# Kernel tuning notes

Hardware: AMD Instinct MI355X
Metric: run time of the kernel (lower is better)

The kernel has to match this reference:

```python
import jax, jax.numpy as jnp
import numpy as np
from jax.scipy.special import ndtri

NUM_BITS = 4
BLOCK_SIZE = 64
OUT_F, IN_F = 4096, 4096


def _nf_table(num_bits=NUM_BITS):
    # Faithful to NFQuantizer.create_normal_map (asymmetric branch)
    offset = 0.9677083
    variations = 2 ** num_bits
    v1 = ndtri(jnp.linspace(offset, 0.5, variations // 2 + 1, dtype=jnp.float32)[:-1])
    v3 = -ndtri(jnp.linspace(offset, 0.5, variations // 2, dtype=jnp.float32)[:-1])
    v = jnp.concatenate([v1, jnp.zeros((1,), jnp.float32), v3])
    v = jnp.sort(v)
    return v / v.max()


def setup_inputs() -> dict:
    key = jax.random.key(0)
    k1, k2, k3, k4, k5 = jax.random.split(key, 5)
    x = jax.random.normal(k1, (8192, IN_F), dtype=jnp.float32)
    qweight = jax.random.randint(k2, (IN_F * OUT_F // 2, 1), 0, 256, dtype=jnp.int32)
    absmax = jax.random.uniform(k3, (IN_F * OUT_F // BLOCK_SIZE, 1), dtype=jnp.float32) * 0.1 + 1e-3
    lora_A = jax.random.normal(k4, (64, IN_F), dtype=jnp.float32) * 0.02
    lora_B = jax.random.normal(k5, (OUT_F, 64), dtype=jnp.float32) * 0.02
    return {"x": x, "qweight": qweight, "absmax": absmax, "lora_A": lora_A, "lora_B": lora_B}


def reference(x, qweight, absmax, lora_A, lora_B):
    table = _nf_table()
    q = qweight[:, 0]
    # dequantize_block: low nibble first (i=0), then high nibble (i=1)
    idx = jnp.stack([q & 0xF, (q >> NUM_BITS) & 0xF], axis=-1)  # [Q, 2]
    w = table[idx].reshape(-1, BLOCK_SIZE) * absmax             # [n_blocks, block_size]
    w = w.reshape(OUT_F, IN_F)
    dense = x @ w.T
    lora = (x @ lora_A.T) @ lora_B.T
    return dense + lora
```

## Files before the change

### kernel.cpp

```cpp
#include <hip/hip_runtime.h>

#define IN_F 4096
#define OUT_F 4096
#define M_ROWS 8192
#define GK 4096

typedef float  floatx4 __attribute__((ext_vector_type(4)));
typedef short  shortx8 __attribute__((ext_vector_type(8)));

__device__ __forceinline__ unsigned short f2bf(float f) {
    unsigned int u = __float_as_uint(f);
    u = (u + 0x7FFFu + ((u >> 16) & 1u)) >> 16;
    return (unsigned short)u;
}

__device__ __forceinline__ float bf2f(unsigned short u) {
    return __uint_as_float((unsigned)u << 16);
}

__constant__ float NF4_TAB[16] = {
    -1.0f, -0.6961928009986877f, -0.5250730514526367f, -0.39491748809814453f,
    -0.28444138169288635f, -0.18477343022823334f, -0.09105003625154495f, 0.0f,
    0.07958029955625534f, 0.16093020141124725f, 0.2461123913526535f, 0.33791524171829224f,
    0.44070982933044434f, 0.5626170039176941f, 0.7229568362236023f, 1.0f
};

__device__ __forceinline__ void gll16(const void* g, void* l) {
    __builtin_amdgcn_global_load_lds(
        (const __attribute__((address_space(1))) void*)g,
        (__attribute__((address_space(3))) void*)l, 16, 0, 0);
}

__global__ __launch_bounds__(256) void prep(
    const float* __restrict__ A, const float* __restrict__ Bm,
    const float* __restrict__ x,
    short* __restrict__ At, short* __restrict__ Bb, short* __restrict__ Xb)
{
    __shared__ float tile[64][65];
    const int b = blockIdx.x;
    const int t = threadIdx.x;

    if (b < 64) {
        const int ib = b * 64;
        const int r = t >> 2, c0 = (t & 3) * 16;
        #pragma unroll
        for (int k = 0; k < 4; ++k) {
            float4 v = *(const float4*)(A + (size_t)r * IN_F + ib + c0 + k * 4);
            tile[r][c0 + k * 4 + 0] = v.x;
            tile[r][c0 + k * 4 + 1] = v.y;
            tile[r][c0 + k * 4 + 2] = v.z;
            tile[r][c0 + k * 4 + 3] = v.w;
        }
        __syncthreads();
        const int i = t >> 2, r0 = (t & 3) * 16;
        union { unsigned short u[8]; int4 v; } p0, p1;
        #pragma unroll
        for (int k = 0; k < 8; ++k) p0.u[k] = f2bf(tile[r0 + k][i]);
        #pragma unroll
        for (int k = 0; k < 8; ++k) p1.u[k] = f2bf(tile[r0 + 8 + k][i]);
        *(int4*)(At + (size_t)(ib + i) * 64 + r0)     = p0.v;
        *(int4*)(At + (size_t)(ib + i) * 64 + r0 + 8) = p1.v;
    } else if (b < 192) {
        const size_t i = ((size_t)(b - 64) * 256 + t) * 8;
        float4 a = *(const float4*)(Bm + i);
        float4 c = *(const float4*)(Bm + i + 4);
        union { unsigned short u[8]; int4 v; } p;
        p.u[0] = f2bf(a.x); p.u[1] = f2bf(a.y); p.u[2] = f2bf(a.z); p.u[3] = f2bf(a.w);
        p.u[4] = f2bf(c.x); p.u[5] = f2bf(c.y); p.u[6] = f2bf(c.z); p.u[7] = f2bf(c.w);
        *(int4*)(Bb + i) = p.v;
    } else {
        const size_t i = ((size_t)(b - 192) * 256 + t) * 8;
        float4 a = *(const float4*)(x + i);
        float4 c = *(const float4*)(x + i + 4);
        union { unsigned short u[8]; int4 v; } p;
        p.u[0] = f2bf(a.x); p.u[1] = f2bf(a.y); p.u[2] = f2bf(a.z); p.u[3] = f2bf(a.w);
        p.u[4] = f2bf(c.x); p.u[5] = f2bf(c.y); p.u[6] = f2bf(c.z); p.u[7] = f2bf(c.w);
        *(int4*)(Xb + i) = p.v;
    }
}

#define BM 128
#define BN 128

__global__ __launch_bounds__(256) void lora_weff(
    const short* __restrict__ Bb,
    const short* __restrict__ At,
    const int*   __restrict__ qw,
    const float* __restrict__ absmax,
    short*       __restrict__ W)
{
    __shared__ union SMem {
        struct { short As[BM * 32]; short Bs[BN * 32]; } mm;
        short Wt[128 * 136];
    } sm;
    __shared__ float nf4s[16];

    const int tid  = threadIdx.x;
    const int lane = tid & 63;
    const int wave = tid >> 6;
    const int bn = blockIdx.x * BN;
    const int bm = blockIdx.y * BM;

    if (tid < 16) nf4s[tid] = NF4_TAB[tid];

    const int r_o = tid >> 1;
    const int h   = tid & 1;
    const int go  = bm + r_o;
    const int* qbase = qw + (size_t)go * 2048 + (bn >> 1) + h * 32;
    int4 q4[8];
    #pragma unroll
    for (int k = 0; k < 8; ++k) q4[k] = *(const int4*)(qbase + 4 * k);
    const float am = absmax[(size_t)go * 64 + (bn >> 6) + h];

    const int ar = tid >> 2;
    const int ac = ((tid & 3) ^ ((ar >> 1) & 3)) * 8;
    const short* gA0 = Bb + (size_t)(bm + ar) * 64 + ac;
    const short* gA1 = gA0 + (size_t)64 * 64;
    const short* gB0 = At + (size_t)(bn + ar) * 64 + ac;
    const short* gB1 = gB0 + (size_t)64 * 64;
    short* lA0 = sm.mm.As + tid * 8;
    short* lA1 = sm.mm.As + 2048 + tid * 8;
    short* lB0 = sm.mm.Bs + tid * 8;
    short* lB1 = sm.mm.Bs + 2048 + tid * 8;

    const int wm = (wave >> 1) * 64;
    const int wn = (wave & 1) * 64;
    const int fr = lane & 15;
    const int qd = lane >> 4;
    const int fk_sw = (((lane >> 4) ^ ((fr >> 1) & 3))) * 8;

    floatx4 zero = {0.f, 0.f, 0.f, 0.f};
    floatx4 acc[4][4];
    #pragma unroll
    for (int i = 0; i < 4; ++i)
        #pragma unroll
        for (int j = 0; j < 4; ++j) acc[i][j] = zero;

    #pragma unroll
    for (int kt = 0; kt < 2; ++kt) {
        gll16(gA0, lA0);
        gll16(gA1, lA1);
        gll16(gB0, lB0);
        gll16(gB1, lB1);
        gA0 += 32; gA1 += 32; gB0 += 32; gB1 += 32;
        __syncthreads();

        shortx8 af[4], bfr[4];
        #pragma unroll
        for (int i = 0; i < 4; ++i) {
            af[i]  = *(const shortx8*)&sm.mm.As[(wm + i * 16 + fr) * 32 + fk_sw];
            bfr[i] = *(const shortx8*)&sm.mm.Bs[(wn + i * 16 + fr) * 32 + fk_sw];
        }
        #pragma unroll
        for (int i = 0; i < 4; ++i)
            #pragma unroll
            for (int j = 0; j < 4; ++j)
                acc[i][j] = __builtin_amdgcn_mfma_f32_16x16x32_bf16(
                    af[i], bfr[j], acc[i][j], 0, 0, 0);
        __syncthreads();
    }

    #pragma unroll
    for (int i = 0; i < 4; ++i) {
        const int r0 = wm + i * 16 + qd * 4;
        #pragma unroll
        for (int j = 0; j < 4; ++j) {
            const int c = wn + j * 16 + fr;
            union { unsigned short u[4]; uint2 v; } p;
            p.u[0] = f2bf(acc[i][j][0]);
            p.u[1] = f2bf(acc[i][j][1]);
            p.u[2] = f2bf(acc[i][j][2]);
            p.u[3] = f2bf(acc[i][j][3]);
            *(uint2*)&sm.Wt[c * 136 + r0] = p.v;
        }
    }
    __syncthreads();

    short* out = W + (size_t)go * IN_F + bn + h * 64;
    #pragma unroll
    for (int k = 0; k < 8; ++k) {
        const int qs[4] = { q4[k].x, q4[k].y, q4[k].z, q4[k].w };
        union { unsigned short u[8]; int4 v; } p;
        #pragma unroll
        for (int d = 0; d < 4; ++d) {
            const int q = qs[d];
            const int c = h * 64 + k * 8 + d * 2;
            const float l0 = bf2f((unsigned short)sm.Wt[c * 136 + r_o]);
            const float l1 = bf2f((unsigned short)sm.Wt[(c + 1) * 136 + r_o]);
            p.u[2 * d]     = f2bf(fmaf(nf4s[q & 15],        am, l0));
            p.u[2 * d + 1] = f2bf(fmaf(nf4s[(q >> 4) & 15], am, l1));
        }
        *(int4*)(out + k * 8) = p.v;
    }
}

#define BK 64

__global__ __launch_bounds__(256) void gemm_bt(
    const short* __restrict__ Xb,
    const short* __restrict__ Wb,
    float*       __restrict__ C)
{
    __shared__ short As[BM * BK];
    __shared__ short Bs[BN * BK];

    const int tid  = threadIdx.x;
    const int lane = tid & 63;
    const int wave = tid >> 6;

    const int orig = blockIdx.y * gridDim.x + blockIdx.x;
    const int xcd  = orig & 7;
    const int t8   = orig >> 3;
    const int bxp  = (xcd & 1) * 16 + (t8 & 15);
    const int byp  = (xcd >> 1) * 16 + (t8 >> 4);
    const int bn = bxp * BN;
    const int bm = byp * BM;

    const int ar  = tid >> 3;
    const int gc  = (tid & 7) ^ (ar & 7);
    const short* gA = Xb + (size_t)(bm + ar) * GK + gc * 8;
    const short* gB = Wb + (size_t)(bn + ar) * GK + gc * 8;
    short* lA = As + tid * 8;
    short* lB = Bs + tid * 8;

    const int wm = (wave >> 1) * 64;
    const int wn = (wave & 1) * 64;
    const int fr = lane & 15;
    const int qd = lane >> 4;
    const int rsw = fr & 7;

    floatx4 zero = {0.f, 0.f, 0.f, 0.f};
    floatx4 acc[4][4];
    #pragma unroll
    for (int i = 0; i < 4; ++i)
        #pragma unroll
        for (int j = 0; j < 4; ++j) acc[i][j] = zero;

    for (int kt = 0; kt < GK / BK; ++kt) {
        #pragma unroll
        for (int r = 0; r < 4; ++r) {
            gll16(gA + (size_t)r * 32 * GK, lA + r * 2048);
            gll16(gB + (size_t)r * 32 * GK, lB + r * 2048);
        }
        gA += BK; gB += BK;
        __syncthreads();

        #pragma unroll
        for (int ks = 0; ks < 2; ++ks) {
            const int p = ((ks * 4 + qd) ^ rsw) * 8;
            shortx8 af[4], bfr[4];
            #pragma unroll
            for (int i = 0; i < 4; ++i) {
                af[i]  = *(const shortx8*)&As[(wm + i * 16 + fr) * BK + p];
                bfr[i] = *(const shortx8*)&Bs[(wn + i * 16 + fr) * BK + p];
            }
            #pragma unroll
            for (int i = 0; i < 4; ++i)
                #pragma unroll
                for (int j = 0; j < 4; ++j)
                    acc[i][j] = __builtin_amdgcn_mfma_f32_16x16x32_bf16(
                        af[i], bfr[j], acc[i][j], 0, 0, 0);
        }
        __syncthreads();
    }

    const int row0 = bm + wm + qd * 4;
    const int col0 = bn + wn + fr;
    #pragma unroll
    for (int i = 0; i < 4; ++i)
        #pragma unroll
        for (int j = 0; j < 4; ++j) {
            float* cp = C + (size_t)(row0 + i * 16) * OUT_F + col0 + j * 16;
            #pragma unroll
            for (int rr = 0; rr < 4; ++rr)
                cp[(size_t)rr * OUT_F] = acc[i][j][rr];
        }
}

extern "C" void kernel_launch(void* const* d_in, const int* in_sizes, int n_in,
                              void* d_out, int out_size, void* d_ws, size_t ws_size,
                              hipStream_t stream) {
    const float* x  = (const float*)d_in[0];
    const int*   qw = (const int*)d_in[1];
    const float* am = (const float*)d_in[2];
    const float* lA = (const float*)d_in[3];
    const float* lB = (const float*)d_in[4];
    float* out = (float*)d_out;

    short* Weff = (short*)d_ws;
    short* Xb   = (short*)((char*)d_ws + (size_t)OUT_F * IN_F * 2);
    short* At   = (short*)((char*)d_ws + (size_t)(OUT_F * IN_F + M_ROWS * IN_F) * 2);
    short* Bb   = At + (size_t)IN_F * 64;

    prep<<<192 + (M_ROWS * IN_F) / 2048, 256, 0, stream>>>(lA, lB, x, At, Bb, Xb);
    lora_weff<<<dim3(IN_F / 128, OUT_F / 128), 256, 0, stream>>>(Bb, At, qw, am, Weff);
    gemm_bt<<<dim3(OUT_F / BN, M_ROWS / BM), 256, 0, stream>>>(Xb, Weff, out);
}
```

Before: 540.5 us.

## Replace GEMM with 256x256 double-buffered 8-wave pipelined kernel

Replaces the 128x128 single-buffered bf16 GEMM with a 256x256-tile kernel that uses 512 threads and a double-buffered 128KB LDS. Global-to-LDS loads for the next one or two K-steps are issued between four MFMA phases. Each phase is separated by explicit barriers, waitcnt calls and setprio hints, so loads and matrix math overlap and each LDS fragment is reused more. The cost is a large LDS footprint that allows only one block per CU, a fragile hand-written vmcnt schedule, and the loss of the previous XCD-aware block remapping.

Measured after the change: 474.9 us. -12.1%, faster.

```diff
diff --git a/kernel.cpp b/kernel.cpp
--- a/kernel.cpp
+++ b/kernel.cpp
@@ -194,80 +194,175 @@
     }
 }
 
-#define BK 64
-
-__global__ __launch_bounds__(256) void gemm_bt(
+#define BM2 256
+#define BN2 256
+#define BK2 64
+#define NT2 (GK / BK2)
+
+#define MFMA16(a, b, c) __builtin_amdgcn_mfma_f32_16x16x32_bf16((a), (b), (c), 0, 0, 0)
+#define SBAR()  __builtin_amdgcn_s_barrier()
+#define SFEN()  __builtin_amdgcn_sched_barrier(0)
+
+__global__ __launch_bounds__(512, 2) void gemm_bt2(
     const short* __restrict__ Xb,
     const short* __restrict__ Wb,
     float*       __restrict__ C)
 {
-    __shared__ short As[BM * BK];
-    __shared__ short Bs[BN * BK];
+    __shared__ short lds[2 * 32768];
 
     const int tid  = threadIdx.x;
     const int lane = tid & 63;
     const int wave = tid >> 6;
-
-    const int orig = blockIdx.y * gridDim.x + blockIdx.x;
-    const int xcd  = orig & 7;
-    const int t8   = orig >> 3;
-    const int bxp  = (xcd & 1) * 16 + (t8 & 15);
-    const int byp  = (xcd >> 1) * 16 + (t8 >> 4);
-    const int bn = bxp * BN;
-    const int bm = byp * BM;
-
-    const int ar  = tid >> 3;
-    const int gc  = (tid & 7) ^ (ar & 7);
-    const short* gA = Xb + (size_t)(bm + ar) * GK + gc * 8;
-    const short* gB = Wb + (size_t)(bn + ar) * GK + gc * 8;
-    short* lA = As + tid * 8;
-    short* lB = Bs + tid * 8;
-
-    const int wm = (wave >> 1) * 64;
-    const int wn = (wave & 1) * 64;
+    const int bn = blockIdx.x * BN2;
+    const int bm = blockIdx.y * BM2;
+
+    const int wm = (wave >> 2) * 128;
+    const int wn = (wave & 3) * 64;
     const int fr = lane & 15;
     const int qd = lane >> 4;
     const int rsw = fr & 7;
+    const int kof[2] = { ((0 * 4 + qd) ^ rsw) << 3, ((1 * 4 + qd) ^ rsw) << 3 };
+
+    const int srow = tid >> 3;
+    const int gch  = (tid & 7) ^ (srow & 7);
+    const short* pA = Xb + (size_t)(bm + srow) * GK + gch * 8;
+    const short* pB = Wb + (size_t)(bn + srow) * GK + gch * 8;
+
+    auto STAGE = [&](const short* P, int matOff, int h, int t, int buf) {
+        short* d = lds + buf * 32768 + matOff + h * 8192 + tid * 8;
+        const short* s = P + (size_t)(h * 128) * GK + (size_t)t * BK2;
+        gll16(s, d);
+        gll16(s + (size_t)64 * GK, d + 4096);
+    };
 
     floatx4 zero = {0.f, 0.f, 0.f, 0.f};
-    floatx4 acc[4][4];
-    #pragma unroll
-    for (int i = 0; i < 4; ++i)
+    floatx4 acc[8][4];
+    #pragma unroll
+    for (int i = 0; i < 8; ++i)
         #pragma unroll
         for (int j = 0; j < 4; ++j) acc[i][j] = zero;
 
-    for (int kt = 0; kt < GK / BK; ++kt) {
-        #pragma unroll
-        for (int r = 0; r < 4; ++r) {
-            gll16(gA + (size_t)r * 32 * GK, lA + r * 2048);
-            gll16(gB + (size_t)r * 32 * GK, lB + r * 2048);
-        }
-        gA += BK; gB += BK;
-        __syncthreads();
-
-        #pragma unroll
-        for (int ks = 0; ks < 2; ++ks) {
-            const int p = ((ks * 4 + qd) ^ rsw) * 8;
-            shortx8 af[4], bfr[4];
-            #pragma unroll
-            for (int i = 0; i < 4; ++i) {
-                af[i]  = *(const shortx8*)&As[(wm + i * 16 + fr) * BK + p];
-                bfr[i] = *(const shortx8*)&Bs[(wn + i * 16 + fr) * BK + p];
+    STAGE(pA, 0,     0, 0, 0);
+    STAGE(pA, 0,     1, 0, 0);
+    STAGE(pB, 16384, 0, 0, 0);
+    STAGE(pB, 16384, 1, 0, 0);
+    STAGE(pA, 0,     0, 1, 1);
+    STAGE(pB, 16384, 0, 1, 1);
+    STAGE(pB, 16384, 1, 1, 1);
+    asm volatile("s_waitcnt vmcnt(6)" ::: "memory");
+    SBAR();
+    SFEN();
+
+    for (int t = 0; t < NT2; ++t) {
+        const int cur = t & 1;
+        const short* Ah = lds + cur * 32768 + (wm >> 7) * 8192;
+        const short* Bh = lds + cur * 32768 + 16384 + (wn >> 7) * 8192;
+        const int bs = wn & 64;
+
+        shortx8 af[4][2], bf[4][2];
+
+        #pragma unroll
+        for (int i = 0; i < 4; ++i) {
+            af[i][0] = *(const shortx8*)(Ah + (i * 16 + fr) * 64 + kof[0]);
+            af[i][1] = *(const shortx8*)(Ah + (i * 16 + fr) * 64 + kof[1]);
+        }
+        #pragma unroll
+        for (int j = 0; j < 2; ++j) {
+            bf[j][0] = *(const shortx8*)(Bh + (bs + j * 16 + fr) * 64 + kof[0]);
+            bf[j][1] = *(const shortx8*)(Bh + (bs + j * 16 + fr) * 64 + kof[1]);
+        }
+        if (t + 1 < NT2) STAGE(pA, 0, 1, t + 1, cur ^ 1);
+        SFEN();
+        SBAR();
+        asm volatile("s_waitcnt lgkmcnt(0)" ::: "memory");
+        SFEN();
+        __builtin_amdgcn_s_setprio(1);
+        #pragma unroll
+        for (int i = 0; i < 4; ++i)
+            #pragma unroll
+            for (int j = 0; j < 2; ++j) {
+                acc[i][j] = MFMA16(af[i][0], bf[j][0], acc[i][j]);
+                acc[i][j] = MFMA16(af[i][1], bf[j][1], acc[i][j]);
             }
-            #pragma unroll
-            for (int i = 0; i < 4; ++i)
-                #pragma unroll
-                for (int j = 0; j < 4; ++j)
-                    acc[i][j] = __builtin_amdgcn_mfma_f32_16x16x32_bf16(
-                        af[i], bfr[j], acc[i][j], 0, 0, 0);
-        }
-        __syncthreads();
+        __builtin_amdgcn_s_setprio(0);
+        SFEN();
+        SBAR();
+        SFEN();
+
+        #pragma unroll
+        for (int j = 0; j < 2; ++j) {
+            bf[2 + j][0] = *(const shortx8*)(Bh + (bs + (2 + j) * 16 + fr) * 64 + kof[0]);
+            bf[2 + j][1] = *(const shortx8*)(Bh + (bs + (2 + j) * 16 + fr) * 64 + kof[1]);
+        }
+        SFEN();
+        SBAR();
+        asm volatile("s_waitcnt lgkmcnt(0)" ::: "memory");
+        SFEN();
+        __builtin_amdgcn_s_setprio(1);
+        #pragma unroll
+        for (int i = 0; i < 4; ++i)
+            #pragma unroll
+            for (int j = 2; j < 4; ++j) {
+                acc[i][j] = MFMA16(af[i][0], bf[j][0], acc[i][j]);
+                acc[i][j] = MFMA16(af[i][1], bf[j][1], acc[i][j]);
+            }
+        __builtin_amdgcn_s_setprio(0);
+        SFEN();
+        SBAR();
+        SFEN();
+
+        #pragma unroll
+        for (int i = 0; i < 4; ++i) {
+            af[i][0] = *(const shortx8*)(Ah + (64 + i * 16 + fr) * 64 + kof[0]);
+            af[i][1] = *(const shortx8*)(Ah + (64 + i * 16 + fr) * 64 + kof[1]);
+        }
+        if (t + 2 < NT2) {
+            STAGE(pB, 16384, 0, t + 2, cur);
+            STAGE(pB, 16384, 1, t + 2, cur);
+        }
+        SFEN();
+        SBAR();
+        asm volatile("s_waitcnt lgkmcnt(0)" ::: "memory");
+        SFEN();
+        __builtin_amdgcn_s_setprio(1);
+        #pragma unroll
+        for (int i = 0; i < 4; ++i)
+            #pragma unroll
+            for (int j = 2; j < 4; ++j) {
+                acc[4 + i][j] = MFMA16(af[i][0], bf[j][0], acc[4 + i][j]);
+                acc[4 + i][j] = MFMA16(af[i][1], bf[j][1], acc[4 + i][j]);
+            }
+        __builtin_amdgcn_s_setprio(0);
+        SFEN();
+        SBAR();
+        SFEN();
+
+        if (t + 2 < NT2) STAGE(pA, 0, 0, t + 2, cur);
+        SFEN();
+        SBAR();
+        __builtin_amdgcn_s_setprio(1);
+        #pragma unroll
+        for (int i = 0; i < 4; ++i)
+            #pragma unroll
+            for (int j = 0; j < 2; ++j) {
+                acc[4 + i][j] = MFMA16(af[i][0], bf[j][0], acc[4 + i][j]);
+                acc[4 + i][j] = MFMA16(af[i][1], bf[j][1], acc[4 + i][j]);
+            }
+        __builtin_amdgcn_s_setprio(0);
+        SFEN();
+        if (t < NT2 - 2) {
+            asm volatile("s_waitcnt vmcnt(6)" ::: "memory");
+        } else if (t == NT2 - 2) {
+            asm volatile("s_waitcnt vmcnt(0)" ::: "memory");
+        }
+        SBAR();
+        SFEN();
     }
 
     const int row0 = bm + wm + qd * 4;
     const int col0 = bn + wn + fr;
     #pragma unroll
-    for (int i = 0; i < 4; ++i)
+    for (int i = 0; i < 8; ++i)
         #pragma unroll
         for (int j = 0; j < 4; ++j) {
             float* cp = C + (size_t)(row0 + i * 16) * OUT_F + col0 + j * 16;
@@ -294,5 +389,5 @@
 
     prep<<<192 + (M_ROWS * IN_F) / 2048, 256, 0, stream>>>(lA, lB, x, At, Bb, Xb);
     lora_weff<<<dim3(IN_F / 128, OUT_F / 128), 256, 0, stream>>>(Bb, At, qw, am, Weff);
-    gemm_bt<<<dim3(OUT_F / BN, M_ROWS / BM), 256, 0, stream>>>(Xb, Weff, out);
-}
+    gemm_bt2<<<dim3(OUT_F / BN2, M_ROWS / BM2), 512, 0, stream>>>(Xb, Weff, out);
+}
```
